# Kernel tuning notes

Hardware: AMD Instinct MI355X
Metric: run time of the kernel (lower is better)

## Reference

```python
import jax, jax.numpy as jnp
import numpy as np

POOLED_H, POOLED_W = 7, 7
SPATIAL_SCALE = 0.0625


def setup_inputs() -> dict:
    key = jax.random.key(0)
    k1, k2, k3, k4, k5, k6, k7 = jax.random.split(key, 7)
    B, C, H, W = 2, 256, 200, 272
    R = 2000
    x = jax.random.normal(k1, (B, C, H, W), dtype=jnp.float32)
    # rois: [batch_idx, cx, cy, w, h, angle_degrees] in image coordinates
    batch_idx = jax.random.randint(k2, (R,), 0, B).astype(jnp.float32)
    cx = jax.random.uniform(k3, (R,), minval=0.0, maxval=W / SPATIAL_SCALE)
    cy = jax.random.uniform(k4, (R,), minval=0.0, maxval=H / SPATIAL_SCALE)
    rw = jax.random.uniform(k5, (R,), minval=32.0, maxval=512.0)
    rh = jax.random.uniform(k6, (R,), minval=32.0, maxval=256.0)
    ang = jax.random.uniform(k7, (R,), minval=-90.0, maxval=90.0)
    rois = jnp.stack([batch_idx, cx, cy, rw, rh, ang], axis=1).astype(jnp.float32)
    return {"input": x, "rois": rois}


def _rround(x):
    # CUDA roundf (half away from zero) ~ floor(x + 0.5) for the positive range used here
    return jnp.floor(x + 0.5)


def reference(input, rois):
    B, C, H, W = input.shape
    batch_idx = rois[:, 0].astype(jnp.int32)          # [R]
    cx = rois[:, 1] * SPATIAL_SCALE
    cy = rois[:, 2] * SPATIAL_SCALE
    rw = rois[:, 3] * SPATIAL_SCALE
    rh = rois[:, 4] * SPATIAL_SCALE
    theta = rois[:, 5] * (jnp.pi / 180.0)

    # Affine transform from pooled-grid coords to feature-map coords (RRPN kernel)
    dx = -POOLED_W / 2.0
    dy = -POOLED_H / 2.0
    Sx = rw / POOLED_W
    Sy = rh / POOLED_H
    ca = jnp.cos(theta)
    sa = jnp.sin(theta)
    M00 = (ca * Sx)[:, None, None]
    M01 = (sa * Sy)[:, None, None]
    M02 = (ca * Sx * dx + sa * Sy * dy + cx)[:, None, None]
    M10 = (-sa * Sx)[:, None, None]
    M11 = (ca * Sy)[:, None, None]
    M12 = (-sa * Sx * dx + ca * Sy * dy + cy)[:, None, None]

    pw = jnp.arange(POOLED_W, dtype=rois.dtype)[None, None, :]   # [1,1,PW]
    ph = jnp.arange(POOLED_H, dtype=rois.dtype)[None, :, None]   # [1,PH,1]

    def corner(a, b):  # bin corner (pw+a, ph+b) -> feature coords, each [R,PH,PW]
        X = M00 * (pw + a) + M01 * (ph + b) + M02
        Y = M10 * (pw + a) + M11 * (ph + b) + M12
        return X, Y

    X0, Y0 = corner(0.0, 0.0)
    X1, Y1 = corner(0.0, 1.0)
    X2, Y2 = corner(1.0, 0.0)
    X3, Y3 = corner(1.0, 1.0)

    leftMost = jnp.maximum(_rround(jnp.minimum(jnp.minimum(X0, X1), jnp.minimum(X2, X3))), 0.0)
    rightMost = jnp.minimum(_rround(jnp.maximum(jnp.maximum(X0, X1), jnp.maximum(X2, X3))), W - 1.0)
    topMost = jnp.maximum(_rround(jnp.minimum(jnp.minimum(Y0, Y1), jnp.minimum(Y2, Y3))), 0.0)
    bottomMost = jnp.minimum(_rround(jnp.maximum(jnp.maximum(Y0, Y1), jnp.maximum(Y2, Y3))), H - 1.0)

    bin_cx = (leftMost + rightMost) / 2.0   # [R,PH,PW]
    bin_cy = (topMost + bottomMost) / 2.0

    bin_l = jnp.floor(bin_cx)
    bin_r = jnp.ceil(bin_cx)
    bin_t = jnp.floor(bin_cy)
    bin_b = jnp.ceil(bin_cy)

    rx = bin_cx - jnp.floor(bin_cx)
    ry = bin_cy - jnp.floor(bin_cy)
    wlt = (1.0 - rx) * (1.0 - ry)
    wrt = rx * (1.0 - ry)
    wrb = rx * ry
    wlb = (1.0 - rx) * ry

    bidx = batch_idx[:, None, None]  # [R,1,1]

    def sample(yy, xx):
        # masked gather of input[b, :, y, x] -> [R,PH,PW,C]
        m = ((yy > -1.0) & (yy < H) & (xx > -1.0) & (xx < W)).astype(input.dtype)
        yi = jnp.clip(yy.astype(jnp.int32), 0, H - 1)
        xi = jnp.clip(xx.astype(jnp.int32), 0, W - 1)
        v = input[bidx, :, yi, xi]  # advanced idx -> [R,PH,PW,C]
        return v * m[..., None]

    lt = sample(bin_t, bin_l)
    rt = sample(bin_t, bin_r)
    lb = sample(bin_b, bin_l)
    rb = sample(bin_b, bin_r)

    out = (lt * wlt[..., None] + rt * wrt[..., None]
           + rb * wrb[..., None] + lb * wlb[..., None])   # [R,PH,PW,C]
    return jnp.transpose(out, (0, 3, 1, 2))                 # [R,C,PH,PW]
```

## Files before the change

kernel.cpp:

```cpp
#include <hip/hip_runtime.h>
#include <math.h>

#define B_   2
#define C_   256
#define H_   200
#define W_   272
#define HW_  (H_*W_)
#define NBIN 49
#define SCALE 0.0625f

__device__ __forceinline__ unsigned short f2bf(float f) {
    union { float f; unsigned int i; } v; v.f = f;
    unsigned int x = v.i;
    return (unsigned short)((x + 0x7FFFu + ((x >> 16) & 1u)) >> 16);
}
__device__ __forceinline__ float bf2f(unsigned int u16) {
    union { unsigned int i; float f; } v; v.i = u16 << 16; return v.f;
}

__device__ __forceinline__ float edge_mask(float yy, float xx) {
    return (yy > -1.0f && yy < (float)H_ && xx > -1.0f && xx < (float)W_) ? 1.0f : 0.0f;
}

__device__ void compute_geom(const float* __restrict__ rois, int r, int bin,
                             int& b, int& yt, int& yb, int& xl, int& xr,
                             float w[4]) {
#pragma clang fp contract(off)
    const float* rp = rois + r * 6;
    b = (int)rp[0];
    float cx = rp[1] * SCALE;
    float cy = rp[2] * SCALE;
    float rw = rp[3] * SCALE;
    float rh = rp[4] * SCALE;
    float theta = rp[5] * (float)(M_PI / 180.0);
    float Sx = rw / 7.0f;
    float Sy = rh / 7.0f;
    double th = (double)theta;
    float ca = (float)cos(th);
    float sa = (float)sin(th);

    float M00 = ca * Sx;
    float M01 = sa * Sy;
    float M02 = (M00 * (-3.5f) + M01 * (-3.5f)) + cx;
    float M10 = (-sa) * Sx;
    float M11 = ca * Sy;
    float M12 = (M10 * (-3.5f) + M11 * (-3.5f)) + cy;

    float pwf = (float)(bin % 7);
    float phf = (float)(bin / 7);
    float x0 = pwf, x1 = pwf + 1.0f;
    float y0 = phf, y1 = phf + 1.0f;

    float X00 = (M00 * x0 + M01 * y0) + M02;
    float X01 = (M00 * x0 + M01 * y1) + M02;
    float X10 = (M00 * x1 + M01 * y0) + M02;
    float X11 = (M00 * x1 + M01 * y1) + M02;
    float Y00 = (M10 * x0 + M11 * y0) + M12;
    float Y01 = (M10 * x0 + M11 * y1) + M12;
    float Y10 = (M10 * x1 + M11 * y0) + M12;
    float Y11 = (M10 * x1 + M11 * y1) + M12;

    float minX = fminf(fminf(X00, X01), fminf(X10, X11));
    float maxX = fmaxf(fmaxf(X00, X01), fmaxf(X10, X11));
    float minY = fminf(fminf(Y00, Y01), fminf(Y10, Y11));
    float maxY = fmaxf(fmaxf(Y00, Y01), fmaxf(Y10, Y11));

    float leftMost   = fmaxf(floorf(minX + 0.5f), 0.0f);
    float rightMost  = fminf(floorf(maxX + 0.5f), (float)(W_ - 1));
    float topMost    = fmaxf(floorf(minY + 0.5f), 0.0f);
    float bottomMost = fminf(floorf(maxY + 0.5f), (float)(H_ - 1));

    float bcx = (leftMost + rightMost) * 0.5f;
    float bcy = (topMost + bottomMost) * 0.5f;
    float fl = floorf(bcx), fr = ceilf(bcx);
    float ft = floorf(bcy), fb = ceilf(bcy);
    float rx = bcx - fl;
    float ry = bcy - ft;

    float wlt = (1.0f - rx) * (1.0f - ry);
    float wrt = rx * (1.0f - ry);
    float wrb = rx * ry;
    float wlb = (1.0f - rx) * ry;

    w[0] = wlt * edge_mask(ft, fl);
    w[1] = wrt * edge_mask(ft, fr);
    w[2] = wlb * edge_mask(fb, fl);
    w[3] = wrb * edge_mask(fb, fr);

    yt = min(max((int)ft, 0), H_ - 1);
    yb = min(max((int)fb, 0), H_ - 1);
    xl = min(max((int)fl, 0), W_ - 1);
    xr = min(max((int)fr, 0), W_ - 1);
}

__global__ __launch_bounds__(256) void transpose_bf16(const float* __restrict__ in,
                                                      unsigned short* __restrict__ outp) {
    __shared__ float tile[64][65];
    int b  = blockIdx.z;
    int p0 = blockIdx.x * 64;
    int c0 = blockIdx.y * 64;
    const float*    ib = in   + (size_t)b * C_ * HW_;
    unsigned short* ob = outp + (size_t)b * HW_ * C_;
    int t = threadIdx.x;

    {
        int col4 = t & 15;
        int row  = t >> 4;
        #pragma unroll
        for (int k = 0; k < 4; k++) {
            int c = row + k * 16;
            float4 v = *(const float4*)(ib + (size_t)(c0 + c) * HW_ + p0 + col4 * 4);
            int p = col4 * 4;
            tile[p + 0][c] = v.x;
            tile[p + 1][c] = v.y;
            tile[p + 2][c] = v.z;
            tile[p + 3][c] = v.w;
        }
    }
    __syncthreads();
    {
        int c8 = t & 7;
        int pr = t >> 3;
        #pragma unroll
        for (int k = 0; k < 2; k++) {
            int p = pr + k * 32;
            ushort4 lo, hi;
            const float* tp = &tile[p][c8 * 8];
            lo.x = f2bf(tp[0]); lo.y = f2bf(tp[1]); lo.z = f2bf(tp[2]); lo.w = f2bf(tp[3]);
            hi.x = f2bf(tp[4]); hi.y = f2bf(tp[5]); hi.z = f2bf(tp[6]); hi.w = f2bf(tp[7]);
            unsigned short* dst = ob + (size_t)(p0 + p) * C_ + c0 + c8 * 8;
            *(ushort4*)(dst)     = lo;
            *(ushort4*)(dst + 4) = hi;
        }
    }
}

__global__ __launch_bounds__(256) void rroi_main_bf16(const unsigned short* __restrict__ xt,
                                                      const float* __restrict__ rois,
                                                      float* __restrict__ outp) {
    __shared__ float lout[C_ * NBIN];
    __shared__ int   goff[NBIN][4];
    __shared__ float gw[NBIN][4];

    int r = blockIdx.x;
    int tid = threadIdx.x;

    if (tid < NBIN) {
        int b, yt, yb, xl, xr; float w[4];
        compute_geom(rois, r, tid, b, yt, yb, xl, xr, w);
        int base = b * HW_ * C_;
        goff[tid][0] = base + (yt * W_ + xl) * C_;
        goff[tid][1] = base + (yt * W_ + xr) * C_;
        goff[tid][2] = base + (yb * W_ + xl) * C_;
        goff[tid][3] = base + (yb * W_ + xr) * C_;
        gw[tid][0] = w[0]; gw[tid][1] = w[1]; gw[tid][2] = w[2]; gw[tid][3] = w[3];
    }
    __syncthreads();

    int lane = tid & 63;
    int wv   = tid >> 6;
    int c4   = lane * 4;

    for (int bin0 = 0; bin0 < NBIN; bin0 += 4) {
        int bin = bin0 + wv;
        if (bin < NBIN) {
            float w0 = gw[bin][0], w1 = gw[bin][1], w2 = gw[bin][2], w3 = gw[bin][3];
            uint2 lt = *(const uint2*)(xt + goff[bin][0] + c4);
            uint2 rt = *(const uint2*)(xt + goff[bin][1] + c4);
            uint2 lb = *(const uint2*)(xt + goff[bin][2] + c4);
            uint2 rb = *(const uint2*)(xt + goff[bin][3] + c4);
            float acc[4];
            {
#pragma clang fp contract(off)
                float a0 = bf2f(lt.x & 0xFFFFu), a1 = bf2f(lt.x >> 16),
                      a2 = bf2f(lt.y & 0xFFFFu), a3 = bf2f(lt.y >> 16);
                float b0 = bf2f(rt.x & 0xFFFFu), b1 = bf2f(rt.x >> 16),
                      b2 = bf2f(rt.y & 0xFFFFu), b3 = bf2f(rt.y >> 16);
                float c0v = bf2f(lb.x & 0xFFFFu), c1v = bf2f(lb.x >> 16),
                      c2v = bf2f(lb.y & 0xFFFFu), c3v = bf2f(lb.y >> 16);
                float d0 = bf2f(rb.x & 0xFFFFu), d1 = bf2f(rb.x >> 16),
                      d2 = bf2f(rb.y & 0xFFFFu), d3 = bf2f(rb.y >> 16);
                acc[0] = ((w0 * a0 + w1 * b0) + w3 * d0) + w2 * c0v;
                acc[1] = ((w0 * a1 + w1 * b1) + w3 * d1) + w2 * c1v;
                acc[2] = ((w0 * a2 + w1 * b2) + w3 * d2) + w2 * c2v;
                acc[3] = ((w0 * a3 + w1 * b3) + w3 * d3) + w2 * c3v;
            }
            #pragma unroll
            for (int jj = 0; jj < 4; jj++) {
                int j = (jj + (lane >> 3)) & 3;
                float v = (j == 0) ? acc[0] : (j == 1) ? acc[1] : (j == 2) ? acc[2] : acc[3];
                lout[(c4 + j) * NBIN + bin] = v;
            }
        }
    }
    __syncthreads();

    float4*       o4 = (float4*)(outp + (size_t)r * (C_ * NBIN));
    const float4* l4 = (const float4*)lout;
    const int n4 = (C_ * NBIN) / 4;
    for (int i = tid; i < n4; i += 256) o4[i] = l4[i];
}

__global__ __launch_bounds__(256) void rroi_main_direct(const float* __restrict__ x,
                                                        const float* __restrict__ rois,
                                                        float* __restrict__ outp) {
    __shared__ float lout[C_ * NBIN];
    __shared__ int   goff[NBIN][4];
    __shared__ float gw[NBIN][4];

    int r = blockIdx.x;
    int tid = threadIdx.x;

    if (tid < NBIN) {
        int b, yt, yb, xl, xr; float w[4];
        compute_geom(rois, r, tid, b, yt, yb, xl, xr, w);
        int base = b * C_ * HW_;
        goff[tid][0] = base + yt * W_ + xl;
        goff[tid][1] = base + yt * W_ + xr;
        goff[tid][2] = base + yb * W_ + xl;
        goff[tid][3] = base + yb * W_ + xr;
        gw[tid][0] = w[0]; gw[tid][1] = w[1]; gw[tid][2] = w[2]; gw[tid][3] = w[3];
    }
    __syncthreads();

    int c = tid;
    int coff = c * HW_;
    for (int bin = 0; bin < NBIN; bin++) {
        float w0 = gw[bin][0], w1 = gw[bin][1], w2 = gw[bin][2], w3 = gw[bin][3];
        float lt = x[goff[bin][0] + coff];
        float rt = x[goff[bin][1] + coff];
        float lb = x[goff[bin][2] + coff];
        float rb = x[goff[bin][3] + coff];
        float v;
        {
#pragma clang fp contract(off)
            v = ((w0 * lt + w1 * rt) + w3 * rb) + w2 * lb;
        }
        lout[c * NBIN + bin] = v;
    }
    __syncthreads();

    float4*       o4 = (float4*)(outp + (size_t)r * (C_ * NBIN));
    const float4* l4 = (const float4*)lout;
    const int n4 = (C_ * NBIN) / 4;
    for (int i = tid; i < n4; i += 256) o4[i] = l4[i];
}

extern "C" void kernel_launch(void* const* d_in, const int* in_sizes, int n_in,
                              void* d_out, int out_size, void* d_ws, size_t ws_size,
                              hipStream_t stream) {
    const float* x    = (const float*)d_in[0];
    const float* rois = (const float*)d_in[1];
    float*       outp = (float*)d_out;
    int R = in_sizes[1] / 6;

    size_t need = (size_t)B_ * HW_ * C_ * sizeof(unsigned short);
    if (ws_size >= need) {
        unsigned short* xt = (unsigned short*)d_ws;
        dim3 g(HW_ / 64, C_ / 64, B_);
        transpose_bf16<<<g, 256, 0, stream>>>(x, xt);
        rroi_main_bf16<<<R, 256, 0, stream>>>(xt, rois, outp);
    } else {
        rroi_main_direct<<<R, 256, 0, stream>>>(x, rois, outp);
    }
}
```

Before: 75.77 us.

## Precompute ROI bin geometry in transpose kernel and prefetch it in main kernel

Bin geometry (corner offsets and bilinear weights) is now computed by an extra slice of blocks in the transpose launch and written to workspace. The main kernel reads it directly and software-prefetches the next bin's geometry, so it no longer runs a per-block trig/geometry phase followed by a barrier. The cost is extra workspace traffic and a hardcoded grid stride of 850 blocks. It also requires a larger workspace, otherwise the slow direct path runs.

```diff
diff --git a/kernel.cpp b/kernel.cpp
--- a/kernel.cpp
+++ b/kernel.cpp
@@ -93,14 +93,41 @@
     xr = min(max((int)fr, 0), W_ - 1);
 }
 
-__global__ __launch_bounds__(256) void transpose_bf16(const float* __restrict__ in,
-                                                      unsigned short* __restrict__ outp) {
+__global__ __launch_bounds__(256) void transpose_geom(const float* __restrict__ in,
+                                                      unsigned short* __restrict__ xt,
+                                                      unsigned int* __restrict__ geom,
+                                                      const float* __restrict__ rois,
+                                                      int R) {
+    if (blockIdx.y == 4) {
+        int total = R * NBIN;
+        for (int gid = (blockIdx.z * 850 + blockIdx.x) * 256 + threadIdx.x;
+             gid < total; gid += 1700 * 256) {
+            int r = gid / NBIN, bin = gid - r * NBIN;
+            int b, yt, yb, xl, xr; float w[4];
+            compute_geom(rois, r, bin, b, yt, yb, xl, xr, w);
+            int base = b * HW_ * C_;
+            uint4 o, wu;
+            o.x = base + (yt * W_ + xl) * C_;
+            o.y = base + (yt * W_ + xr) * C_;
+            o.z = base + (yb * W_ + xl) * C_;
+            o.w = base + (yb * W_ + xr) * C_;
+            wu.x = __float_as_uint(w[0]);
+            wu.y = __float_as_uint(w[1]);
+            wu.z = __float_as_uint(w[2]);
+            wu.w = __float_as_uint(w[3]);
+            uint4* gp = (uint4*)(geom + (size_t)gid * 8);
+            gp[0] = o;
+            gp[1] = wu;
+        }
+        return;
+    }
+
     __shared__ float tile[64][65];
     int b  = blockIdx.z;
     int p0 = blockIdx.x * 64;
     int c0 = blockIdx.y * 64;
-    const float*    ib = in   + (size_t)b * C_ * HW_;
-    unsigned short* ob = outp + (size_t)b * HW_ * C_;
+    const float*    ib = in + (size_t)b * C_ * HW_;
+    unsigned short* ob = xt + (size_t)b * HW_ * C_;
     int t = threadIdx.x;
 
     {
@@ -136,62 +163,57 @@
 }
 
 __global__ __launch_bounds__(256) void rroi_main_bf16(const unsigned short* __restrict__ xt,
-                                                      const float* __restrict__ rois,
+                                                      const unsigned int* __restrict__ geom,
                                                       float* __restrict__ outp) {
     __shared__ float lout[C_ * NBIN];
-    __shared__ int   goff[NBIN][4];
-    __shared__ float gw[NBIN][4];
-
-    int r = blockIdx.x;
-    int tid = threadIdx.x;
-
-    if (tid < NBIN) {
-        int b, yt, yb, xl, xr; float w[4];
-        compute_geom(rois, r, tid, b, yt, yb, xl, xr, w);
-        int base = b * HW_ * C_;
-        goff[tid][0] = base + (yt * W_ + xl) * C_;
-        goff[tid][1] = base + (yt * W_ + xr) * C_;
-        goff[tid][2] = base + (yb * W_ + xl) * C_;
-        goff[tid][3] = base + (yb * W_ + xr) * C_;
-        gw[tid][0] = w[0]; gw[tid][1] = w[1]; gw[tid][2] = w[2]; gw[tid][3] = w[3];
-    }
-    __syncthreads();
-
+
+    int r    = blockIdx.x;
+    int tid  = threadIdx.x;
     int lane = tid & 63;
     int wv   = tid >> 6;
     int c4   = lane * 4;
 
-    for (int bin0 = 0; bin0 < NBIN; bin0 += 4) {
-        int bin = bin0 + wv;
-        if (bin < NBIN) {
-            float w0 = gw[bin][0], w1 = gw[bin][1], w2 = gw[bin][2], w3 = gw[bin][3];
-            uint2 lt = *(const uint2*)(xt + goff[bin][0] + c4);
-            uint2 rt = *(const uint2*)(xt + goff[bin][1] + c4);
-            uint2 lb = *(const uint2*)(xt + goff[bin][2] + c4);
-            uint2 rb = *(const uint2*)(xt + goff[bin][3] + c4);
-            float acc[4];
-            {
+    const uint4* gb = (const uint4*)(geom + (size_t)r * NBIN * 8);
+
+    int bin = wv;
+    uint4 go = gb[2 * bin];
+    uint4 gu = gb[2 * bin + 1];
+    while (bin < NBIN) {
+        int nbin = bin + 4;
+        uint4 ngo, ngu;
+        if (nbin < NBIN) {
+            ngo = gb[2 * nbin];
+            ngu = gb[2 * nbin + 1];
+        }
+        float w0 = __uint_as_float(gu.x), w1 = __uint_as_float(gu.y);
+        float w2 = __uint_as_float(gu.z), w3 = __uint_as_float(gu.w);
+        uint2 lt = *(const uint2*)(xt + go.x + c4);
+        uint2 rt = *(const uint2*)(xt + go.y + c4);
+        uint2 lb = *(const uint2*)(xt + go.z + c4);
+        uint2 rb = *(const uint2*)(xt + go.w + c4);
+        float acc[4];
+        {
 #pragma clang fp contract(off)
-                float a0 = bf2f(lt.x & 0xFFFFu), a1 = bf2f(lt.x >> 16),
-                      a2 = bf2f(lt.y & 0xFFFFu), a3 = bf2f(lt.y >> 16);
-                float b0 = bf2f(rt.x & 0xFFFFu), b1 = bf2f(rt.x >> 16),
-                      b2 = bf2f(rt.y & 0xFFFFu), b3 = bf2f(rt.y >> 16);
-                float c0v = bf2f(lb.x & 0xFFFFu), c1v = bf2f(lb.x >> 16),
-                      c2v = bf2f(lb.y & 0xFFFFu), c3v = bf2f(lb.y >> 16);
-                float d0 = bf2f(rb.x & 0xFFFFu), d1 = bf2f(rb.x >> 16),
-                      d2 = bf2f(rb.y & 0xFFFFu), d3 = bf2f(rb.y >> 16);
-                acc[0] = ((w0 * a0 + w1 * b0) + w3 * d0) + w2 * c0v;
-                acc[1] = ((w0 * a1 + w1 * b1) + w3 * d1) + w2 * c1v;
-                acc[2] = ((w0 * a2 + w1 * b2) + w3 * d2) + w2 * c2v;
-                acc[3] = ((w0 * a3 + w1 * b3) + w3 * d3) + w2 * c3v;
-            }
-            #pragma unroll
-            for (int jj = 0; jj < 4; jj++) {
-                int j = (jj + (lane >> 3)) & 3;
-                float v = (j == 0) ? acc[0] : (j == 1) ? acc[1] : (j == 2) ? acc[2] : acc[3];
-                lout[(c4 + j) * NBIN + bin] = v;
-            }
-        }
+            float a0 = bf2f(lt.x & 0xFFFFu), a1 = bf2f(lt.x >> 16),
+                  a2 = bf2f(lt.y & 0xFFFFu), a3 = bf2f(lt.y >> 16);
+            float b0 = bf2f(rt.x & 0xFFFFu), b1 = bf2f(rt.x >> 16),
+                  b2 = bf2f(rt.y & 0xFFFFu), b3 = bf2f(rt.y >> 16);
+            float c0v = bf2f(lb.x & 0xFFFFu), c1v = bf2f(lb.x >> 16),
+                  c2v = bf2f(lb.y & 0xFFFFu), c3v = bf2f(lb.y >> 16);
+            float d0 = bf2f(rb.x & 0xFFFFu), d1 = bf2f(rb.x >> 16),
+                  d2 = bf2f(rb.y & 0xFFFFu), d3 = bf2f(rb.y >> 16);
+            acc[0] = ((w0 * a0 + w1 * b0) + w3 * d0) + w2 * c0v;
+            acc[1] = ((w0 * a1 + w1 * b1) + w3 * d1) + w2 * c1v;
+            acc[2] = ((w0 * a2 + w1 * b2) + w3 * d2) + w2 * c2v;
+            acc[3] = ((w0 * a3 + w1 * b3) + w3 * d3) + w2 * c3v;
+        }
+        #pragma unroll
+        for (int jj = 0; jj < 4; jj++) {
+            int j = (jj + (lane >> 3)) & 3;
+            float v = (j == 0) ? acc[0] : (j == 1) ? acc[1] : (j == 2) ? acc[2] : acc[3];
+            lout[(c4 + j) * NBIN + bin] = v;
+        }
+        go = ngo; gu = ngu; bin = nbin;
     }
     __syncthreads();
 
@@ -240,10 +262,10 @@
     }
     __syncthreads();
 
-    float4*       o4 = (float4*)(outp + (size_t)r * (C_ * NBIN));
-    const float4* l4 = (const float4*)lout;
+    float* o = outp + (size_t)r * (C_ * NBIN);
     const int n4 = (C_ * NBIN) / 4;
-    for (int i = tid; i < n4; i += 256) o4[i] = l4[i];
+    for (int i = tid; i < n4; i += 256)
+        *(float4*)(o + i * 4) = *(const float4*)(&lout[i * 4]);
 }
 
 extern "C" void kernel_launch(void* const* d_in, const int* in_sizes, int n_in,
@@ -254,12 +276,14 @@
     float*       outp = (float*)d_out;
     int R = in_sizes[1] / 6;
 
-    size_t need = (size_t)B_ * HW_ * C_ * sizeof(unsigned short);
+    size_t geom_off = 64ull * 1024 * 1024;
+    size_t need = geom_off + (size_t)R * NBIN * 8 * sizeof(unsigned int);
     if (ws_size >= need) {
-        unsigned short* xt = (unsigned short*)d_ws;
-        dim3 g(HW_ / 64, C_ / 64, B_);
-        transpose_bf16<<<g, 256, 0, stream>>>(x, xt);
-        rroi_main_bf16<<<R, 256, 0, stream>>>(xt, rois, outp);
+        unsigned short* xt   = (unsigned short*)d_ws;
+        unsigned int*   geom = (unsigned int*)((char*)d_ws + geom_off);
+        dim3 g(HW_ / 64, 5, B_);
+        transpose_geom<<<g, 256, 0, stream>>>(x, xt, geom, rois, R);
+        rroi_main_bf16<<<R, 256, 0, stream>>>(xt, geom, outp);
     } else {
         rroi_main_direct<<<R, 256, 0, stream>>>(x, rois, outp);
     }
```

Measured after the change: 76.98 us. No clear change (+1.6%).
